# Optimization experiments

Measured on AMD Instinct MI355X. Metric: run time of the kernel, lower is better.

Reference implementation:

```python
import jax, jax.numpy as jnp
import numpy as np

LX, LY = 16, 16
N = 2 * LX * LY        # 512 lattice sites (sequence length)
NH = 128               # GRU hidden size
K = 2                  # binary occupation categories
NS = 4096              # number of Monte-Carlo samples (batch)


def setup_inputs() -> dict:
    key = jax.random.key(0)
    k0, k1, k2, k3 = jax.random.split(key, 4)
    gru_kernel = jax.random.normal(k0, (K, 3 * NH), jnp.float32) * (1.0 / np.sqrt(K))
    gru_rkernel = jax.random.normal(k1, (NH, 3 * NH), jnp.float32) * (1.0 / np.sqrt(NH))
    gru_bias = jnp.zeros((2, 3 * NH), jnp.float32)  # [input_bias; recurrent_bias] (reset_after=True)
    dense_w = jax.random.normal(k2, (NH, K), jnp.float32) * (1.0 / np.sqrt(NH))
    dense_b = jnp.zeros((K,), jnp.float32)
    u = jax.random.uniform(k3, (NS, N), jnp.float32)  # pre-drawn noise for categorical draws
    return {"gru_kernel": gru_kernel, "gru_rkernel": gru_rkernel, "gru_bias": gru_bias,
            "dense_w": dense_w, "dense_b": dense_b, "u": u}


def reference(gru_kernel, gru_rkernel, gru_bias, dense_w, dense_b, u):
    """Autoregressive GRU sampling over N lattice sites.
    Returns (samples [ns,N] int32, log_prob [ns] float32)."""
    ns = u.shape[0]
    b_in, b_rec = gru_bias[0], gru_bias[1]

    def step(carry, u_t):
        h, x = carry                       # h: [ns,NH], x: one-hot prev sample [ns,K]
        xg = x @ gru_kernel + b_in          # [ns,3NH]
        hg = h @ gru_rkernel + b_rec        # [ns,3NH]
        xz, xr, xh = jnp.split(xg, 3, axis=-1)   # keras gate order: z, r, h
        hz, hr, hh = jnp.split(hg, 3, axis=-1)
        z = jax.nn.sigmoid(xz + hz)
        r = jax.nn.sigmoid(xr + hr)
        hc = jnp.tanh(xh + r * hh)          # reset_after=True candidate
        h_new = z * h + (1.0 - z) * hc
        probs = jax.nn.softmax(h_new @ dense_w + dense_b, axis=-1)  # [ns,K]
        p1 = probs[:, 1]
        s = (u_t < p1).astype(jnp.int32)    # categorical draw (K=2) via inverse CDF
        logp_t = jnp.log(jnp.where(s == 1, p1, probs[:, 0]) + 1e-10)
        x_new = jax.nn.one_hot(s, K, dtype=h.dtype)
        return (h_new, x_new), (s, logp_t)

    h0 = jnp.zeros((ns, NH), u.dtype)
    x0 = jnp.zeros((ns, K), u.dtype)        # zero input at first site
    (_, _), (samples, logps) = jax.lax.scan(step, (h0, x0), u.T)  # scan over N sites
    return samples.T, logps.sum(axis=0)
```

## Files before the change

### kernel.cpp

```cpp
#include <hip/hip_runtime.h>

#define NHID   128
#define NSTEPS 512
#define NSAMP  4096
#define SPB    16
#define BS     512
#define NBLK   (NSAMP / SPB)
#define KL4    17
#define SAMP_ELEMS (NSAMP * NSTEPS)
#define WT_ELEMS   (3 * NHID * NHID)

typedef float v2f __attribute__((ext_vector_type(2)));
typedef float v4f __attribute__((ext_vector_type(4)));

static __device__ __forceinline__ v2f fma2(v2f a, v2f b, v2f c) {
#if defined(__has_builtin)
#if __has_builtin(__builtin_elementwise_fma)
    return __builtin_elementwise_fma(a, b, c);
#else
    return (v2f){fmaf(a.x, b.x, c.x), fmaf(a.y, b.y, c.y)};
#endif
#else
    return (v2f){fmaf(a.x, b.x, c.x), fmaf(a.y, b.y, c.y)};
#endif
}

__global__ __launch_bounds__(256)
void pack_w_kernel(const float* __restrict__ rk, float* __restrict__ wt) {
    const int i = blockIdx.x * 256 + threadIdx.x;
    if (i < WT_ELEMS) {
        const int j  = i & 3;
        const int c  = (i >> 2) & 127;
        const int k4 = (i >> 9) & 31;
        const int g  = i >> 14;
        wt[i] = rk[(k4 * 4 + j) * 384 + g * NHID + c];
    }
}

template<int TR>
__global__ __launch_bounds__(BS, 1)
void vmc_gru_kernel(const float* __restrict__ gk,
                    const float* __restrict__ rk,
                    const float* __restrict__ gb,
                    const float* __restrict__ dw,
                    const float* __restrict__ db,
                    const float* __restrict__ u,
                    const float* __restrict__ wt,
                    float* __restrict__ out)
{
    __shared__ float  hsm[2][NHID][SPB];
    __shared__ float  part[2][8][SPB][2];
    __shared__ float  uld[NSTEPS][SPB];
    __shared__ float4 slds[3 * KL4 * NHID];

    const int tid = threadIdx.x;
    const int cg  = tid >> 2;
    const int sq  = tid & 3;
    const int s0  = sq * 4;
    const int wv  = tid >> 6;

    {
        const int sl = tid >> 5;
        const int t0 = (tid & 31) * 16;
        const float* up = u + (size_t)(blockIdx.x * SPB + sl) * NSTEPS + t0;
        const float4 a = ((const float4*)up)[0];
        const float4 b = ((const float4*)up)[1];
        const float4 c = ((const float4*)up)[2];
        const float4 d = ((const float4*)up)[3];
        const float tmp[16] = {a.x,a.y,a.z,a.w, b.x,b.y,b.z,b.w,
                               c.x,c.y,c.z,c.w, d.x,d.y,d.z,d.w};
        #pragma unroll
        for (int i = 0; i < 16; ++i) uld[t0 + i][sl] = tmp[i];
    }
    if (TR) {
        const float4* wt4 = (const float4*)wt;
        for (int i = tid; i < 3 * KL4 * NHID; i += BS) {
            const int g  = i / (KL4 * NHID);
            const int r  = i - g * (KL4 * NHID);
            slds[i] = wt4[g * 4096 + r];
        }
    }
    for (int i = tid; i < NHID * SPB; i += BS) (&hsm[0][0][0])[i] = 0.0f;
    __syncthreads();

    const float brz = gb[384 + cg];
    const float brr = gb[384 + 128 + cg];
    const float brh = gb[384 + 256 + cg];
    const float xzI = gb[cg],       xz0c = xzI + gk[cg],       xz1c = xzI + gk[384 + cg];
    const float xrI = gb[128 + cg], xr0c = xrI + gk[128 + cg], xr1c = xrI + gk[384 + 128 + cg];
    const float xhI = gb[256 + cg], xh0c = xhI + gk[256 + cg], xh1c = xhI + gk[384 + 256 + cg];
    const float dwc0 = dw[cg * 2], dwc1 = dw[cg * 2 + 1];
    const float db0 = db[0], db1 = db[1];

    const v4f* lz = (const v4f*)slds + cg;
    const v4f* lr = (const v4f*)slds + KL4 * 128 + cg;
    const v4f* lh = (const v4f*)slds + 2 * KL4 * 128 + cg;
    const v4f* wz4 = (const v4f*)wt + cg;
    const v4f* wr4 = (const v4f*)wt + 4096 + cg;
    const v4f* wh4 = (const v4f*)wt + 8192 + cg;
    const float* rkp = rk + cg;

    int   pv[4] = {0, 0, 0, 0};
    float lg[4] = {0.f, 0.f, 0.f, 0.f};
    int cur = 0;

    for (int t = 0; t < NSTEPS; ++t) {
        v2f az01 = {brz, brz}, az23 = {brz, brz};
        v2f ar01 = {brr, brr}, ar23 = {brr, brr};
        v2f ah01 = {brh, brh}, ah23 = {brh, brh};

#define GEMM_K4(WZ, WR, WH, K4) do {                                        \
    const v4f h_0 = *(const v4f*)&hsm[cur][4*(K4)+0][s0];                   \
    const v4f h_1 = *(const v4f*)&hsm[cur][4*(K4)+1][s0];                   \
    const v4f h_2 = *(const v4f*)&hsm[cur][4*(K4)+2][s0];                   \
    const v4f hh[4] = {h_0, h_1, h_2, *(const v4f*)&hsm[cur][4*(K4)+3][s0]};\
    _Pragma("unroll")                                                        \
    for (int kk = 0; kk < 4; ++kk) {                                         \
        const v2f hlo = hh[kk].xy;                                           \
        const v2f hhi = hh[kk].zw;                                           \
        const v2f wz2 = {(WZ)[kk], (WZ)[kk]};                                \
        const v2f wr2 = {(WR)[kk], (WR)[kk]};                                \
        const v2f wh2 = {(WH)[kk], (WH)[kk]};                                \
        az01 = fma2(wz2, hlo, az01); az23 = fma2(wz2, hhi, az23);            \
        ar01 = fma2(wr2, hlo, ar01); ar23 = fma2(wr2, hhi, ar23);            \
        ah01 = fma2(wh2, hlo, ah01); ah23 = fma2(wh2, hhi, ah23);            \
    }                                                                         \
} while (0)

        if (TR) {
            #pragma unroll 4
            for (int k4 = 0; k4 < KL4; ++k4) {
                const v4f wz = lz[k4 * 128];
                const v4f wr = lr[k4 * 128];
                const v4f wh = lh[k4 * 128];
                GEMM_K4(wz, wr, wh, k4);
            }
            #pragma unroll 4
            for (int k4 = KL4; k4 < 32; ++k4) {
                const v4f wz = wz4[k4 * 128];
                const v4f wr = wr4[k4 * 128];
                const v4f wh = wh4[k4 * 128];
                GEMM_K4(wz, wr, wh, k4);
            }
        } else {
            const float* wp = rkp;
            #pragma unroll 4
            for (int k = 0; k < NHID; ++k) {
                const float wz = wp[0];
                const float wr = wp[NHID];
                const float wh = wp[2 * NHID];
                const v4f hv = *(const v4f*)&hsm[cur][k][s0];
                const v2f hlo = hv.xy, hhi = hv.zw;
                const v2f wz2 = {wz, wz}, wr2 = {wr, wr}, wh2 = {wh, wh};
                az01 = fma2(wz2, hlo, az01); az23 = fma2(wz2, hhi, az23);
                ar01 = fma2(wr2, hlo, ar01); ar23 = fma2(wr2, hhi, ar23);
                ah01 = fma2(wh2, hlo, ah01); ah23 = fma2(wh2, hhi, ah23);
                wp += 3 * NHID;
            }
        }
#undef GEMM_K4

        const float az[4] = {az01.x, az01.y, az23.x, az23.y};
        const float ar[4] = {ar01.x, ar01.y, ar23.x, ar23.y};
        const float ah[4] = {ah01.x, ah01.y, ah23.x, ah23.y};

        const v4f ho = *(const v4f*)&hsm[cur][cg][s0];
        const float hov[4] = {ho.x, ho.y, ho.z, ho.w};
        float hn[4], p0s[4], p1s[4];
        #pragma unroll
        for (int j = 0; j < 4; ++j) {
            float xz = pv[j] ? xz1c : xz0c;
            float xr = pv[j] ? xr1c : xr0c;
            float xh = pv[j] ? xh1c : xh0c;
            if (t == 0) { xz = xzI; xr = xrI; xh = xhI; }
            const float z  = 1.0f / (1.0f + expf(-(xz + az[j])));
            const float r  = 1.0f / (1.0f + expf(-(xr + ar[j])));
            const float hc = tanhf(xh + r * ah[j]);
            const float hnew = z * hov[j] + (1.0f - z) * hc;
            hn[j] = hnew;
            p0s[j] = hnew * dwc0;
            p1s[j] = hnew * dwc1;
        }
        *(v4f*)&hsm[cur ^ 1][cg][s0] = (v4f){hn[0], hn[1], hn[2], hn[3]};

        #pragma unroll
        for (int off = 4; off < 64; off <<= 1) {
            #pragma unroll
            for (int j = 0; j < 4; ++j) {
                p0s[j] += __shfl_xor(p0s[j], off);
                p1s[j] += __shfl_xor(p1s[j], off);
            }
        }
        const int pb = t & 1;
        if ((tid & 63) < 4) {
            *(float4*)&part[pb][wv][s0][0]     = make_float4(p0s[0], p1s[0], p0s[1], p1s[1]);
            *(float4*)&part[pb][wv][s0 + 2][0] = make_float4(p0s[2], p1s[2], p0s[3], p1s[3]);
        }
        __syncthreads();

        float l0[4] = {db0, db0, db0, db0};
        float l1[4] = {db1, db1, db1, db1};
        #pragma unroll
        for (int w = 0; w < 8; ++w) {
            const float4 qa = *(const float4*)&part[pb][w][s0][0];
            const float4 qb = *(const float4*)&part[pb][w][s0 + 2][0];
            l0[0] += qa.x; l1[0] += qa.y;
            l0[1] += qa.z; l1[1] += qa.w;
            l0[2] += qb.x; l1[2] += qb.y;
            l0[3] += qb.z; l1[3] += qb.w;
        }
        const float4 uu = *(const float4*)&uld[t][s0];
        const float uv[4] = {uu.x, uu.y, uu.z, uu.w};
        #pragma unroll
        for (int j = 0; j < 4; ++j) {
            const float mx = fmaxf(l0[j], l1[j]);
            const float e0 = expf(l0[j] - mx);
            const float e1 = expf(l1[j] - mx);
            const float inv = 1.0f / (e0 + e1);
            const float p1v = e1 * inv;
            const int st = (uv[j] < p1v) ? 1 : 0;
            const float psel = st ? p1v : (e0 * inv);
            lg[j] += logf(psel + 1e-10f);
            pv[j] = st;
            if (cg == 0)
                out[(size_t)(blockIdx.x * SPB + s0 + j) * NSTEPS + t] = (float)st;
        }
        cur ^= 1;
    }

    if (cg == 0) {
        #pragma unroll
        for (int j = 0; j < 4; ++j)
            out[SAMP_ELEMS + blockIdx.x * SPB + s0 + j] = lg[j];
    }
}

extern "C" void kernel_launch(void* const* d_in, const int* in_sizes, int n_in,
                              void* d_out, int out_size, void* d_ws, size_t ws_size,
                              hipStream_t stream) {
    const float* gk = (const float*)d_in[0];
    const float* rk = (const float*)d_in[1];
    const float* gb = (const float*)d_in[2];
    const float* dw = (const float*)d_in[3];
    const float* db = (const float*)d_in[4];
    const float* u  = (const float*)d_in[5];
    float* out = (float*)d_out;

    if (ws_size >= (size_t)WT_ELEMS * sizeof(float)) {
        float* wt = (float*)d_ws;
        pack_w_kernel<<<(WT_ELEMS + 255) / 256, 256, 0, stream>>>(rk, wt);
        vmc_gru_kernel<1><<<NBLK, BS, 0, stream>>>(gk, rk, gb, dw, db, u, wt, out);
    } else {
        vmc_gru_kernel<0><<<NBLK, BS, 0, stream>>>(gk, rk, gb, dw, db, u, rk, out);
    }
}
```

Measured before the change: 4.228 ms.

## Use inline packed FMA asm, ds_swizzle reductions, batched log, two-block occupancy

```diff
diff --git a/kernel.cpp b/kernel.cpp
--- a/kernel.cpp
+++ b/kernel.cpp
@@ -13,16 +13,16 @@
 typedef float v2f __attribute__((ext_vector_type(2)));
 typedef float v4f __attribute__((ext_vector_type(4)));
 
-static __device__ __forceinline__ v2f fma2(v2f a, v2f b, v2f c) {
-#if defined(__has_builtin)
-#if __has_builtin(__builtin_elementwise_fma)
-    return __builtin_elementwise_fma(a, b, c);
-#else
-    return (v2f){fmaf(a.x, b.x, c.x), fmaf(a.y, b.y, c.y)};
-#endif
-#else
-    return (v2f){fmaf(a.x, b.x, c.x), fmaf(a.y, b.y, c.y)};
-#endif
+#define PK_LO(ACC, W2, H2) \
+    asm("v_pk_fma_f32 %0, %1, %2, %0 op_sel:[0,0,0] op_sel_hi:[0,1,1]" \
+        : "+v"(ACC) : "v"(W2), "v"(H2))
+#define PK_HI(ACC, W2, H2) \
+    asm("v_pk_fma_f32 %0, %1, %2, %0 op_sel:[1,0,0] op_sel_hi:[1,1,1]" \
+        : "+v"(ACC) : "v"(W2), "v"(H2))
+
+template<int IMM>
+__device__ __forceinline__ float swz(float x) {
+    return __int_as_float(__builtin_amdgcn_ds_swizzle(__float_as_int(x), IMM));
 }
 
 __global__ __launch_bounds__(256)
@@ -38,7 +38,7 @@
 }
 
 template<int TR>
-__global__ __launch_bounds__(BS, 1)
+__global__ __launch_bounds__(BS, 2)
 void vmc_gru_kernel(const float* __restrict__ gk,
                     const float* __restrict__ rk,
                     const float* __restrict__ gb,
@@ -48,10 +48,10 @@
                     const float* __restrict__ wt,
                     float* __restrict__ out)
 {
-    __shared__ float  hsm[2][NHID][SPB];
-    __shared__ float  part[2][8][SPB][2];
-    __shared__ float  uld[NSTEPS][SPB];
-    __shared__ float4 slds[3 * KL4 * NHID];
+    __shared__ float hsm[2][NHID][SPB];
+    __shared__ float part[2][8][SPB][2];
+    __shared__ float uld[NSTEPS][SPB];
+    __shared__ v4f   slds[3 * KL4 * NHID];
 
     const int tid = threadIdx.x;
     const int cg  = tid >> 2;
@@ -73,10 +73,10 @@
         for (int i = 0; i < 16; ++i) uld[t0 + i][sl] = tmp[i];
     }
     if (TR) {
-        const float4* wt4 = (const float4*)wt;
+        const v4f* wt4 = (const v4f*)wt;
         for (int i = tid; i < 3 * KL4 * NHID; i += BS) {
-            const int g  = i / (KL4 * NHID);
-            const int r  = i - g * (KL4 * NHID);
+            const int g = i / (KL4 * NHID);
+            const int r = i - g * (KL4 * NHID);
             slds[i] = wt4[g * 4096 + r];
         }
     }
@@ -92,9 +92,9 @@
     const float dwc0 = dw[cg * 2], dwc1 = dw[cg * 2 + 1];
     const float db0 = db[0], db1 = db[1];
 
-    const v4f* lz = (const v4f*)slds + cg;
-    const v4f* lr = (const v4f*)slds + KL4 * 128 + cg;
-    const v4f* lh = (const v4f*)slds + 2 * KL4 * 128 + cg;
+    const v4f* lz = slds + cg;
+    const v4f* lr = slds + KL4 * 128 + cg;
+    const v4f* lh = slds + 2 * KL4 * 128 + cg;
     const v4f* wz4 = (const v4f*)wt + cg;
     const v4f* wr4 = (const v4f*)wt + 4096 + cg;
     const v4f* wh4 = (const v4f*)wt + 8192 + cg;
@@ -102,29 +102,35 @@
 
     int   pv[4] = {0, 0, 0, 0};
     float lg[4] = {0.f, 0.f, 0.f, 0.f};
+    float pr[4] = {1.f, 1.f, 1.f, 1.f};
     int cur = 0;
 
     for (int t = 0; t < NSTEPS; ++t) {
         v2f az01 = {brz, brz}, az23 = {brz, brz};
         v2f ar01 = {brr, brr}, ar23 = {brr, brr};
         v2f ah01 = {brh, brh}, ah23 = {brh, brh};
-
-#define GEMM_K4(WZ, WR, WH, K4) do {                                        \
-    const v4f h_0 = *(const v4f*)&hsm[cur][4*(K4)+0][s0];                   \
-    const v4f h_1 = *(const v4f*)&hsm[cur][4*(K4)+1][s0];                   \
-    const v4f h_2 = *(const v4f*)&hsm[cur][4*(K4)+2][s0];                   \
-    const v4f hh[4] = {h_0, h_1, h_2, *(const v4f*)&hsm[cur][4*(K4)+3][s0]};\
-    _Pragma("unroll")                                                        \
-    for (int kk = 0; kk < 4; ++kk) {                                         \
-        const v2f hlo = hh[kk].xy;                                           \
-        const v2f hhi = hh[kk].zw;                                           \
-        const v2f wz2 = {(WZ)[kk], (WZ)[kk]};                                \
-        const v2f wr2 = {(WR)[kk], (WR)[kk]};                                \
-        const v2f wh2 = {(WH)[kk], (WH)[kk]};                                \
-        az01 = fma2(wz2, hlo, az01); az23 = fma2(wz2, hhi, az23);            \
-        ar01 = fma2(wr2, hlo, ar01); ar23 = fma2(wr2, hhi, ar23);            \
-        ah01 = fma2(wh2, hlo, ah01); ah23 = fma2(wh2, hhi, ah23);            \
-    }                                                                         \
+        const float* hb = &hsm[cur][0][0];
+
+#define GEMM_K4(WZ, WR, WH, K4) do {                                      \
+    const v4f h0 = *(const v4f*)(hb + (4*(K4)+0)*SPB + s0);               \
+    const v4f h1 = *(const v4f*)(hb + (4*(K4)+1)*SPB + s0);               \
+    const v4f h2 = *(const v4f*)(hb + (4*(K4)+2)*SPB + s0);               \
+    const v4f h3 = *(const v4f*)(hb + (4*(K4)+3)*SPB + s0);               \
+    const v2f wzA = (WZ).xy, wzB = (WZ).zw;                               \
+    const v2f wrA = (WR).xy, wrB = (WR).zw;                               \
+    const v2f whA = (WH).xy, whB = (WH).zw;                               \
+    PK_LO(az01, wzA, h0.xy); PK_LO(az23, wzA, h0.zw);                     \
+    PK_LO(ar01, wrA, h0.xy); PK_LO(ar23, wrA, h0.zw);                     \
+    PK_LO(ah01, whA, h0.xy); PK_LO(ah23, whA, h0.zw);                     \
+    PK_HI(az01, wzA, h1.xy); PK_HI(az23, wzA, h1.zw);                     \
+    PK_HI(ar01, wrA, h1.xy); PK_HI(ar23, wrA, h1.zw);                     \
+    PK_HI(ah01, whA, h1.xy); PK_HI(ah23, whA, h1.zw);                     \
+    PK_LO(az01, wzB, h2.xy); PK_LO(az23, wzB, h2.zw);                     \
+    PK_LO(ar01, wrB, h2.xy); PK_LO(ar23, wrB, h2.zw);                     \
+    PK_LO(ah01, whB, h2.xy); PK_LO(ah23, whB, h2.zw);                     \
+    PK_HI(az01, wzB, h3.xy); PK_HI(az23, wzB, h3.zw);                     \
+    PK_HI(ar01, wrB, h3.xy); PK_HI(ar23, wrB, h3.zw);                     \
+    PK_HI(ah01, whB, h3.xy); PK_HI(ah23, whB, h3.zw);                     \
 } while (0)
 
         if (TR) {
@@ -135,7 +141,7 @@
                 const v4f wh = lh[k4 * 128];
                 GEMM_K4(wz, wr, wh, k4);
             }
-            #pragma unroll 4
+            #pragma unroll
             for (int k4 = KL4; k4 < 32; ++k4) {
                 const v4f wz = wz4[k4 * 128];
                 const v4f wr = wr4[k4 * 128];
@@ -146,15 +152,23 @@
             const float* wp = rkp;
             #pragma unroll 4
             for (int k = 0; k < NHID; ++k) {
-                const float wz = wp[0];
-                const float wr = wp[NHID];
-                const float wh = wp[2 * NHID];
-                const v4f hv = *(const v4f*)&hsm[cur][k][s0];
-                const v2f hlo = hv.xy, hhi = hv.zw;
-                const v2f wz2 = {wz, wz}, wr2 = {wr, wr}, wh2 = {wh, wh};
-                az01 = fma2(wz2, hlo, az01); az23 = fma2(wz2, hhi, az23);
-                ar01 = fma2(wr2, hlo, ar01); ar23 = fma2(wr2, hhi, ar23);
-                ah01 = fma2(wh2, hlo, ah01); ah23 = fma2(wh2, hhi, ah23);
+                const float wzs = wp[0];
+                const float wrs = wp[NHID];
+                const float whs = wp[2 * NHID];
+                const v4f hv = *(const v4f*)(hb + k * SPB + s0);
+                const float hk[4] = {hv.x, hv.y, hv.z, hv.w};
+                float azs[4] = {az01.x, az01.y, az23.x, az23.y};
+                float ars[4] = {ar01.x, ar01.y, ar23.x, ar23.y};
+                float ahs[4] = {ah01.x, ah01.y, ah23.x, ah23.y};
+                #pragma unroll
+                for (int j = 0; j < 4; ++j) azs[j] = fmaf(wzs, hk[j], azs[j]);
+                #pragma unroll
+                for (int j = 0; j < 4; ++j) ars[j] = fmaf(wrs, hk[j], ars[j]);
+                #pragma unroll
+                for (int j = 0; j < 4; ++j) ahs[j] = fmaf(whs, hk[j], ahs[j]);
+                az01 = (v2f){azs[0], azs[1]}; az23 = (v2f){azs[2], azs[3]};
+                ar01 = (v2f){ars[0], ars[1]}; ar23 = (v2f){ars[2], ars[3]};
+                ah01 = (v2f){ahs[0], ahs[1]}; ah23 = (v2f){ahs[2], ahs[3]};
                 wp += 3 * NHID;
             }
         }
@@ -164,7 +178,7 @@
         const float ar[4] = {ar01.x, ar01.y, ar23.x, ar23.y};
         const float ah[4] = {ah01.x, ah01.y, ah23.x, ah23.y};
 
-        const v4f ho = *(const v4f*)&hsm[cur][cg][s0];
+        const v4f ho = *(const v4f*)(hb + cg * SPB + s0);
         const float hov[4] = {ho.x, ho.y, ho.z, ho.w};
         float hn[4], p0s[4], p1s[4];
         #pragma unroll
@@ -184,12 +198,12 @@
         *(v4f*)&hsm[cur ^ 1][cg][s0] = (v4f){hn[0], hn[1], hn[2], hn[3]};
 
         #pragma unroll
-        for (int off = 4; off < 64; off <<= 1) {
-            #pragma unroll
-            for (int j = 0; j < 4; ++j) {
-                p0s[j] += __shfl_xor(p0s[j], off);
-                p1s[j] += __shfl_xor(p1s[j], off);
-            }
+        for (int j = 0; j < 4; ++j) {
+            p0s[j] += swz<0x101F>(p0s[j]);  p1s[j] += swz<0x101F>(p1s[j]);
+            p0s[j] += swz<0x201F>(p0s[j]);  p1s[j] += swz<0x201F>(p1s[j]);
+            p0s[j] += swz<0x401F>(p0s[j]);  p1s[j] += swz<0x401F>(p1s[j]);
+            p0s[j] += __shfl_xor(p0s[j], 32);
+            p1s[j] += __shfl_xor(p1s[j], 32);
         }
         const int pb = t & 1;
         if ((tid & 63) < 4) {
@@ -220,10 +234,14 @@
             const float p1v = e1 * inv;
             const int st = (uv[j] < p1v) ? 1 : 0;
             const float psel = st ? p1v : (e0 * inv);
-            lg[j] += logf(psel + 1e-10f);
+            pr[j] *= (psel + 1e-10f);
             pv[j] = st;
             if (cg == 0)
                 out[(size_t)(blockIdx.x * SPB + s0 + j) * NSTEPS + t] = (float)st;
+        }
+        if ((t & 7) == 7) {
+            #pragma unroll
+            for (int j = 0; j < 4; ++j) { lg[j] += logf(pr[j]); pr[j] = 1.0f; }
         }
         cur ^= 1;
     }
```

New measurement: 3.743 ms. 11.5% less time.
